# Kernel tuning notes

Hardware: AMD Instinct MI355X
Metric: run time of the kernel (lower is better)

Reference implementation:

```python
import jax, jax.numpy as jnp
import numpy as np
import math

N = 20000      # nodes
E = 320000     # edges
D = 256        # in_dim == out_dim (residual requires equality)
H = 8          # heads
K = D // H     # k_dim = 32
T = 3          # node types
R = 5          # edge (relation) types
C = 16         # output classes
SQRT_K = math.sqrt(K)


def setup_inputs() -> dict:
    key = jax.random.key(0)
    ks = jax.random.split(key, 18)
    x = jax.random.normal(ks[0], (N, D), jnp.float32)
    edge_index = jax.random.randint(ks[1], (2, E), 0, N, jnp.int32)
    node_type = jax.random.randint(ks[2], (N,), 0, T, jnp.int32)
    edge_type = jax.random.randint(ks[3], (E,), 0, R, jnp.int32)
    g_lin = math.sqrt(2.0 / (D + D))
    g_rel = math.sqrt(2.0 / (K + K))
    g_out = math.sqrt(2.0 / (D + C))
    Wk = jax.random.normal(ks[4], (T, D, D), jnp.float32) * g_lin
    bk = jnp.zeros((T, D), jnp.float32)
    Wq = jax.random.normal(ks[5], (T, D, D), jnp.float32) * g_lin
    bq = jnp.zeros((T, D), jnp.float32)
    Wv = jax.random.normal(ks[6], (T, D, D), jnp.float32) * g_lin
    bv = jnp.zeros((T, D), jnp.float32)
    Wa = jax.random.normal(ks[7], (T, D, D), jnp.float32) * g_lin
    ba = jnp.zeros((T, D), jnp.float32)
    rel_prior = jnp.ones((R, H), jnp.float32)
    rel_att = jax.random.normal(ks[8], (R, H, K, K), jnp.float32) * g_rel
    rel_msg = jax.random.normal(ks[9], (R, H, K, K), jnp.float32) * g_rel
    W_out = jax.random.normal(ks[10], (D, C), jnp.float32) * g_out
    b_out = jnp.zeros((C,), jnp.float32)
    return {"x": x, "edge_index": edge_index, "node_type": node_type,
            "edge_type": edge_type, "Wk": Wk, "bk": bk, "Wq": Wq, "bq": bq,
            "Wv": Wv, "bv": bv, "Wa": Wa, "ba": ba, "rel_prior": rel_prior,
            "rel_att": rel_att, "rel_msg": rel_msg, "W_out": W_out, "b_out": b_out}


def _typed_linear(h, W, b, node_type):
    # per-node-type Linear: small fixed loop over T types, masked select
    out = jnp.zeros((h.shape[0], W.shape[2]), h.dtype)
    for t in range(T):
        m = (node_type == t)[:, None]
        out = out + jnp.where(m, h @ W[t] + b[t], 0.0)
    return out


def _hgt_forward(x, edge_index, node_type, edge_type, Wk, bk, Wq, bq, Wv, bv,
                 Wa, ba, rel_prior, rel_att, rel_msg, W_out, b_out):
    src, dst = edge_index[0], edge_index[1]
    # typed projections -> [N, H, K]
    Kn = _typed_linear(x, Wk, bk, node_type).reshape(N, H, K)
    Qn = _typed_linear(x, Wq, bq, node_type).reshape(N, H, K)
    Vn = _typed_linear(x, Wv, bv, node_type).reshape(N, H, K)
    Ke, Qe, Ve = Kn[src], Qn[dst], Vn[src]  # [E, H, K] gathers
    # relation-specific bilinear transforms of K and V (fixed loop over R)
    Kt = jnp.zeros_like(Ke)
    Mt = jnp.zeros_like(Ve)
    for r in range(R):
        m = (edge_type == r)[:, None, None]
        Kt = Kt + jnp.where(m, jnp.einsum('ehk,hkl->ehl', Ke, rel_att[r]), 0.0)
        Mt = Mt + jnp.where(m, jnp.einsum('ehk,hkl->ehl', Ve, rel_msg[r]), 0.0)
    # attention logits with relation prior, scaled by sqrt(k_dim)
    logits = (Qe * Kt).sum(-1) * rel_prior[edge_type] / SQRT_K  # [E, H]
    # segment softmax over incoming edges per destination node
    mx = jax.ops.segment_max(logits, dst, num_segments=N)       # [N, H]
    ex = jnp.exp(logits - mx[dst])
    sm = jax.ops.segment_sum(ex, dst, num_segments=N)           # [N, H]
    att = ex / sm[dst]                                          # [E, H]
    # weighted messages, scatter-add aggregation
    msg = (Mt * att[:, :, None]).reshape(E, D)
    aggr = jax.ops.segment_sum(msg, dst, num_segments=N)        # [N, D]
    # update: ELU, typed output linear, residual
    h = jax.nn.elu(aggr)
    h = _typed_linear(h, Wa, ba, node_type) + x
    # final classifier + log_softmax
    return jax.nn.log_softmax(h @ W_out + b_out, axis=1)


def reference(x, edge_index, node_type, edge_type, Wk, bk, Wq, bq, Wv, bv,
              Wa, ba, rel_prior, rel_att, rel_msg, W_out, b_out):
    return _hgt_forward(x, edge_index, node_type, edge_type, Wk, bk, Wq, bq,
                        Wv, bv, Wa, ba, rel_prior, rel_att, rel_msg, W_out, b_out)
```

## Files before the change

### kernel.cpp

```cpp
#include <hip/hip_runtime.h>
#include <hip/hip_bf16.h>
#include <math.h>

#define NN 20000
#define NE 320000
#define DD 256
#define NH 8
#define KK 32
#define NR 5
#define NC 16
#define NB2 391
#define NPAD 20096

typedef unsigned short u16;
typedef unsigned int u32;
typedef __attribute__((ext_vector_type(8))) short bf16x8;
typedef __attribute__((ext_vector_type(4))) float f32x4;

__device__ __forceinline__ float bf2f(u16 v){ return __uint_as_float(((u32)v)<<16); }
__device__ __forceinline__ u16 f2bf(float f){
  u32 u = __float_as_uint(f);
  return (u16)((u + 0x7FFFu + ((u>>16)&1u)) >> 16);
}

__global__ void k_pre1(const int* __restrict__ ntype, const int* __restrict__ ei,
                       const int* __restrict__ etype, int* __restrict__ cnt,
                       int* __restrict__ off2, int* __restrict__ perm){
  int b = blockIdx.x;
  if(b < 79){
    int n = b*256 + threadIdx.x;
    int t = (n < NN) ? ntype[n] : -1;
    int lane = threadIdx.x & 63;
    #pragma unroll
    for(int tt=0; tt<3; tt++){
      unsigned long long mask = __ballot(t == tt);
      int leader = __ffsll((long long)mask) - 1;
      if(lane == leader) atomicAdd(&cnt[tt], __popcll(mask));
    }
  } else if(b < 1329){
    int e = (b-79)*256 + threadIdx.x;
    if(e < NE) atomicAdd(&off2[ei[NE + e]*NR + etype[e]], 1);
  } else {
    int i = (b-1329)*256 + threadIdx.x;
    if(i < NPAD) perm[i] = -1;
  }
}

__global__ __launch_bounds__(256) void k_pre2(int* __restrict__ off2, int* __restrict__ bsum,
                                              const int* __restrict__ cnt, int* __restrict__ boff){
  if(blockIdx.x == NB2){
    if(threadIdx.x == 0){
      int a = (cnt[0]+31)&~31;
      int bb = (cnt[1]+31)&~31;
      boff[0]=0; boff[1]=a; boff[2]=a+bb;
    }
    return;
  }
  __shared__ int sh[256];
  int t = threadIdx.x;
  int i = blockIdx.x*256 + t;
  int v = (i < NN*NR) ? off2[i] : 0;
  sh[t] = v;
  __syncthreads();
  for(int off=1; off<256; off<<=1){
    int val = (t >= off) ? sh[t-off] : 0;
    __syncthreads();
    sh[t] += val;
    __syncthreads();
  }
  if(i < NN*NR) off2[i] = sh[t] - v;
  if(t == 255) bsum[blockIdx.x] = sh[255];
}
__global__ __launch_bounds__(512) void k_scan2(int* __restrict__ bsum, int* __restrict__ off2){
  __shared__ int sh[512];
  int t = threadIdx.x;
  int v = (t < NB2) ? bsum[t] : 0;
  sh[t] = v;
  __syncthreads();
  for(int off=1; off<512; off<<=1){
    int val = (t >= off) ? sh[t-off] : 0;
    __syncthreads();
    sh[t] += val;
    __syncthreads();
  }
  if(t < NB2) bsum[t] = sh[t] - v;
  if(t == 511) off2[NN*NR] = sh[511];
}
__global__ void k_pre3(int* __restrict__ off2, const int* __restrict__ bsum,
                       const int* __restrict__ ntype, const int* __restrict__ boff,
                       int* __restrict__ bcur, int* __restrict__ perm,
                       int* __restrict__ pos2){
  int b = blockIdx.x;
  if(b < NB2){
    int i = b*256 + threadIdx.x;
    if(i < NN*NR) off2[i] += bsum[b];
  } else {
    int n = (b-NB2)*256 + threadIdx.x;
    int t = (n < NN) ? ntype[n] : -1;
    int lane = threadIdx.x & 63;
    #pragma unroll
    for(int tt=0; tt<3; tt++){
      unsigned long long mask = __ballot(t == tt);
      if(t == tt){
        int rank = __popcll(mask & ((1ull<<lane)-1ull));
        int leader = __ffsll((long long)mask) - 1;
        int base = 0;
        if(lane == leader) base = atomicAdd(&bcur[tt], __popcll(mask));
        base = __shfl(base, leader);
        int p = boff[tt] + base + rank;
        perm[p] = n;
        pos2[n] = p;
      }
    }
  }
}

__global__ __launch_bounds__(256) void k_work1(
    const int* __restrict__ ei, const int* __restrict__ etype,
    int* __restrict__ off2, int* __restrict__ packed,
    const int* __restrict__ pos2,
    const float* __restrict__ x, u16* __restrict__ xb,
    const float* __restrict__ Wk, const float* __restrict__ Wq,
    const float* __restrict__ Wv, const float* __restrict__ Wa,
    u16* __restrict__ Wtk, u16* __restrict__ Wtq,
    u16* __restrict__ Wtv, u16* __restrict__ Wta,
    const float* __restrict__ rmsg, const float* __restrict__ ratt,
    const float* __restrict__ prior, const float* __restrict__ Wo,
    u16* __restrict__ Mtm, u16* __restrict__ Atb, u16* __restrict__ Wot)
{
  __shared__ float tile[32][33];
  int b = blockIdx.x;
  if(b < 1250){
    int e = b*256 + threadIdx.x;
    if(e < NE){
      int pos = atomicAdd(&off2[ei[NE+e]*NR + etype[e]], 1);
      packed[pos] = pos2[ei[e]];
    }
  } else if(b < 3750){
    int i = (b-1250)*256 + threadIdx.x;
    float4 v0 = ((const float4*)x)[i*2+0];
    float4 v1 = ((const float4*)x)[i*2+1];
    uint4 o;
    o.x = (u32)f2bf(v0.x) | ((u32)f2bf(v0.y)<<16);
    o.y = (u32)f2bf(v0.z) | ((u32)f2bf(v0.w)<<16);
    o.z = (u32)f2bf(v1.x) | ((u32)f2bf(v1.y)<<16);
    o.w = (u32)f2bf(v1.z) | ((u32)f2bf(v1.w)<<16);
    ((uint4*)xb)[i] = o;
  } else if(b < 4518){
    int bp = b - 3750;
    int bx = bp & 7, by = (bp>>3) & 7, z = bp >> 6;
    int tensor = z/3, t = z%3;
    const float* W = (tensor==0) ? Wk : (tensor==1) ? Wq : (tensor==2) ? Wv : Wa;
    u16* O = (tensor==0) ? Wtk : (tensor==1) ? Wtq : (tensor==2) ? Wtv : Wta;
    int i0 = bx*32, j0 = by*32;
    int rr = threadIdx.x>>5, cc = threadIdx.x&31;
    #pragma unroll
    for(int p=0;p<4;p++)
      tile[rr+p*8][cc] = W[t*65536 + (i0+rr+p*8)*256 + j0+cc];
    __syncthreads();
    #pragma unroll
    for(int p=0;p<4;p++)
      O[t*65536 + (j0+rr+p*8)*256 + i0+cc] = f2bf(tile[cc][rr+p*8]);
  } else {
    int bp = b - 4518;
    if(bp < 160){
      int idx = bp*256 + threadIdx.x;
      int l = idx & 31, k = (idx >> 5) & 31, rh = idx >> 10;
      Mtm[(rh*32 + l)*32 + k] = f2bf(rmsg[idx]);
    } else if(bp < 320){
      int idx = (bp-160)*256 + threadIdx.x;
      int rh = idx >> 10;
      float scale = prior[rh] * 0.17677669529663687f;
      Atb[idx] = f2bf(ratt[idx] * scale);
    } else {
      int idx = (bp-320)*256 + threadIdx.x;
      int c = idx & 15, k = idx >> 4;
      Wot[c*DD + k] = f2bf(Wo[k*NC + c]);
    }
  }
}

#define XSP 264
__global__ __launch_bounds__(256) void k_projqa(
    const u16* __restrict__ xb, const int* __restrict__ perm, const int* __restrict__ boff,
    const u16* __restrict__ Wtk, const u16* __restrict__ Wtq, const u16* __restrict__ Wtv,
    const float* __restrict__ bk, const float* __restrict__ bq, const float* __restrict__ bv,
    u16* __restrict__ KVn, u16* __restrict__ Qn)
{
  __shared__ u16 smem[32*XSP];
  __shared__ int gids[32];
  int tid = threadIdx.x;
  int ts = (blockIdx.x >> 1)*32;
  int cb = (blockIdx.x & 1)*128;
  int t = (ts >= boff[2]) ? 2 : (ts >= boff[1]) ? 1 : 0;
  if(tid < 32) gids[tid] = perm[ts + tid];
  __syncthreads();
  #pragma unroll
  for(int it=0; it<4; it++){
    int q = tid + it*256;
    int row = q >> 5, c = q & 31;
    int g = gids[row];
    uint4 v = make_uint4(0,0,0,0);
    if(g >= 0) v = ((const uint4*)(xb + (size_t)g*DD))[c];
    ((uint4*)(smem + row*XSP))[c] = v;
  }
  __syncthreads();
  int lane = tid & 63;
  int w = tid >> 6;
  int quad = lane >> 4;
  int l16 = lane & 15;
  f32x4 accK[2][2], accQ[2][2], accV[2][2];
  #pragma unroll
  for(int mt=0;mt<2;mt++)
    #pragma unroll
    for(int nt=0;nt<2;nt++){
      accK[mt][nt]=(f32x4)(0.f); accQ[mt][nt]=(f32x4)(0.f); accV[mt][nt]=(f32x4)(0.f);
    }
  const u16* wkp = Wtk + (size_t)t*65536;
  const u16* wqp = Wtq + (size_t)t*65536;
  const u16* wvp = Wtv + (size_t)t*65536;
  #pragma unroll
  for(int kk=0; kk<8; kk++){
    int kb = kk*32 + quad*8;
    bf16x8 a0 = *(const bf16x8*)(smem + l16*XSP + kb);
    bf16x8 a1 = *(const bf16x8*)(smem + (16+l16)*XSP + kb);
    #pragma unroll
    for(int nt=0; nt<2; nt++){
      int n = cb + w*32 + nt*16 + l16;
      bf16x8 bK = *(const bf16x8*)(wkp + (size_t)n*DD + kb);
      bf16x8 bQ = *(const bf16x8*)(wqp + (size_t)n*DD + kb);
      bf16x8 bV = *(const bf16x8*)(wvp + (size_t)n*DD + kb);
      accK[0][nt] = __builtin_amdgcn_mfma_f32_16x16x32_bf16(a0, bK, accK[0][nt], 0,0,0);
      accK[1][nt] = __builtin_amdgcn_mfma_f32_16x16x32_bf16(a1, bK, accK[1][nt], 0,0,0);
      accQ[0][nt] = __builtin_amdgcn_mfma_f32_16x16x32_bf16(a0, bQ, accQ[0][nt], 0,0,0);
      accQ[1][nt] = __builtin_amdgcn_mfma_f32_16x16x32_bf16(a1, bQ, accQ[1][nt], 0,0,0);
      accV[0][nt] = __builtin_amdgcn_mfma_f32_16x16x32_bf16(a0, bV, accV[0][nt], 0,0,0);
      accV[1][nt] = __builtin_amdgcn_mfma_f32_16x16x32_bf16(a1, bV, accV[1][nt], 0,0,0);
    }
  }
  __syncthreads();
  #pragma unroll
  for(int nt=0; nt<2; nt++){
    int lc = w*32 + nt*16 + l16;
    int colg = cb + lc;
    int kvo = ((lc >> 2)*8 + (lc & 3));
    float bkv = bk[t*DD+colg], bvv = bv[t*DD+colg];
    #pragma unroll
    for(int mt=0; mt<2; mt++){
      #pragma unroll
      for(int reg=0; reg<4; reg++){
        int row = mt*16 + quad*4 + reg;
        smem[row*XSP + kvo]     = f2bf(accK[mt][nt][reg] + bkv);
        smem[row*XSP + kvo + 4] = f2bf(accV[mt][nt][reg] + bvv);
      }
    }
  }
  __syncthreads();
  #pragma unroll
  for(int it=0; it<4; it++){
    int q = tid + it*256;
    int row = q >> 5, c = q & 31;
    *(uint4*)(KVn + (size_t)(ts+row)*512 + (cb>>2)*8 + c*8) = ((uint4*)(smem + row*XSP))[c];
  }
  __syncthreads();
  #pragma unroll
  for(int nt=0; nt<2; nt++){
    int lc = w*32 + nt*16 + l16;
    float bqv = bq[t*DD + cb + lc];
    #pragma unroll
    for(int mt=0; mt<2; mt++){
      #pragma unroll
      for(int reg=0; reg<4; reg++){
        int row = mt*16 + quad*4 + reg;
        smem[row*XSP + lc] = f2bf(accQ[mt][nt][reg] + bqv);
      }
    }
  }
  __syncthreads();
  #pragma unroll
  for(int it=0; it<2; it++){
    int q = tid + it*256;
    int row = q >> 4, c = q & 15;
    *(uint4*)(Qn + (size_t)(ts+row)*DD + cb + c*8) = ((uint4*)(smem + row*XSP))[c];
  }
}

#define QSP 264
__global__ __launch_bounds__(256) void k_qa(
    const u16* __restrict__ Qn, const u16* __restrict__ Atb, u16* __restrict__ QA)
{
  __shared__ u16 qs[32*QSP];
  int tid = threadIdx.x;
  int tile = blockIdx.x / NR;
  int r = blockIdx.x - tile*NR;
  int ts = tile*32;
  #pragma unroll
  for(int it=0; it<4; it++){
    int q = tid + it*256;
    int row = q >> 5, c = q & 31;
    ((uint4*)(qs + row*QSP))[c] = ((const uint4*)(Qn + (size_t)(ts+row)*DD))[c];
  }
  __syncthreads();
  int lane = tid & 63, w = tid >> 6, quad = lane >> 4, l16 = lane & 15;
  f32x4 acc[2][2][2];
  #pragma unroll
  for(int hh=0;hh<2;hh++)
    #pragma unroll
    for(int mt=0;mt<2;mt++)
      #pragma unroll
      for(int nt=0;nt<2;nt++) acc[hh][mt][nt]=(f32x4)(0.f);
  #pragma unroll
  for(int hh=0; hh<2; hh++){
    int h = w*2 + hh;
    bf16x8 a0 = *(const bf16x8*)(qs + l16*QSP + h*32 + quad*8);
    bf16x8 a1 = *(const bf16x8*)(qs + (16+l16)*QSP + h*32 + quad*8);
    const u16* ap = Atb + (size_t)(r*NH + h)*1024;
    bf16x8 b0 = *(const bf16x8*)(ap + l16*32 + quad*8);
    bf16x8 b1 = *(const bf16x8*)(ap + (16+l16)*32 + quad*8);
    acc[hh][0][0] = __builtin_amdgcn_mfma_f32_16x16x32_bf16(a0, b0, acc[hh][0][0], 0,0,0);
    acc[hh][0][1] = __builtin_amdgcn_mfma_f32_16x16x32_bf16(a0, b1, acc[hh][0][1], 0,0,0);
    acc[hh][1][0] = __builtin_amdgcn_mfma_f32_16x16x32_bf16(a1, b0, acc[hh][1][0], 0,0,0);
    acc[hh][1][1] = __builtin_amdgcn_mfma_f32_16x16x32_bf16(a1, b1, acc[hh][1][1], 0,0,0);
  }
  __syncthreads();
  #pragma unroll
  for(int hh=0; hh<2; hh++){
    int h = w*2 + hh;
    #pragma unroll
    for(int mt=0; mt<2; mt++)
      #pragma unroll
      for(int nt=0; nt<2; nt++)
        #pragma unroll
        for(int reg=0; reg<4; reg++){
          int row = mt*16 + quad*4 + reg;
          qs[row*QSP + h*32 + nt*16 + l16] = f2bf(acc[hh][mt][nt][reg]);
        }
  }
  __syncthreads();
  #pragma unroll
  for(int it=0; it<4; it++){
    int q = tid + it*256;
    int row = q >> 5, c = q & 31;
    *(uint4*)(QA + ((size_t)(ts+row)*NR + r)*DD + c*8) = ((uint4*)(qs + row*QSP))[c];
  }
}

#define VSP 264
__global__ __launch_bounds__(256) void k_edge(
    const u16* __restrict__ KVn, const u16* __restrict__ QA,
    const int* __restrict__ off2, const int* __restrict__ packed,
    const int* __restrict__ perm, u16* __restrict__ aggrV)
{
  int lane = threadIdx.x & 63;
  int p = blockIdx.x*4 + (threadIdx.x >> 6);
  if(p >= NPAD) return;
  int n = perm[p];
  if(n < 0) return;
  int off = lane*4;
  float4 qa[NR];
  {
    const u16* qp = QA + (size_t)p*NR*DD + off;
    #pragma unroll
    for(int r=0;r<NR;r++){
      ushort4 q = *(const ushort4*)(qp + r*DD);
      qa[r] = make_float4(bf2f(q.x),bf2f(q.y),bf2f(q.z),bf2f(q.w));
    }
  }
  int eb[NR+1];
  eb[0] = (n==0) ? 0 : off2[n*NR - 1];
  #pragma unroll
  for(int i=1;i<=NR;i++) eb[i] = off2[n*NR + i - 1];
  float4 acc[NR];
  float s = 0.f;
  int lo8 = lane*8;

  #define EDGE_DOT(kv, q, dd) \
    { float k0=__uint_as_float((kv).x<<16), k1=__uint_as_float((kv).x&0xffff0000u); \
      float k2=__uint_as_float((kv).y<<16), k3=__uint_as_float((kv).y&0xffff0000u); \
      dd = k0*(q).x + k1*(q).y + k2*(q).z + k3*(q).w; }
  #define EDGE_ACC(kv, p, a) \
    { float v0=__uint_as_float((kv).z<<16), v1=__uint_as_float((kv).z&0xffff0000u); \
      float v2=__uint_as_float((kv).w<<16), v3=__uint_as_float((kv).w&0xffff0000u); \
      (a).x += (p)*v0; (a).y += (p)*v1; (a).z += (p)*v2; (a).w += (p)*v3; }
  #define RED3(d) { d += __shfl_xor(d,1); d += __shfl_xor(d,2); d += __shfl_xor(d,4); }

  #pragma unroll
  for(int r=0;r<NR;r++){
    float4 q = qa[r];
    float4 a = make_float4(0.f,0.f,0.f,0.f);
    int e = eb[r], end = eb[r+1];
    for(; e+4 <= end; e += 4){
      int s0 = packed[e], s1 = packed[e+1], s2 = packed[e+2], s3 = packed[e+3];
      uint4 kv0 = *(const uint4*)(KVn + (size_t)s0*512 + lo8);
      uint4 kv1 = *(const uint4*)(KVn + (size_t)s1*512 + lo8);
      uint4 kv2 = *(const uint4*)(KVn + (size_t)s2*512 + lo8);
      uint4 kv3 = *(const uint4*)(KVn + (size_t)s3*512 + lo8);
      float d0,d1,d2,d3;
      EDGE_DOT(kv0,q,d0); EDGE_DOT(kv1,q,d1); EDGE_DOT(kv2,q,d2); EDGE_DOT(kv3,q,d3);
      RED3(d0); RED3(d1); RED3(d2); RED3(d3);
      float p0=__expf(d0), p1=__expf(d1), p2=__expf(d2), p3=__expf(d3);
      s += p0 + p1 + p2 + p3;
      EDGE_ACC(kv0,p0,a); EDGE_ACC(kv1,p1,a); EDGE_ACC(kv2,p2,a); EDGE_ACC(kv3,p3,a);
    }
    if(e+2 <= end){
      int s0 = packed[e], s1 = packed[e+1];
      uint4 kv0 = *(const uint4*)(KVn + (size_t)s0*512 + lo8);
      uint4 kv1 = *(const uint4*)(KVn + (size_t)s1*512 + lo8);
      float d0,d1;
      EDGE_DOT(kv0,q,d0); EDGE_DOT(kv1,q,d1);
      RED3(d0); RED3(d1);
      float p0=__expf(d0), p1=__expf(d1);
      s += p0 + p1;
      EDGE_ACC(kv0,p0,a); EDGE_ACC(kv1,p1,a);
      e += 2;
    }
    if(e < end){
      int s0 = packed[e];
      uint4 kv0 = *(const uint4*)(KVn + (size_t)s0*512 + lo8);
      float d0;
      EDGE_DOT(kv0,q,d0);
      RED3(d0);
      float p0=__expf(d0);
      s += p0;
      EDGE_ACC(kv0,p0,a);
    }
    acc[r] = a;
  }
  #undef EDGE_DOT
  #undef EDGE_ACC
  #undef RED3
  float inv = (s > 0.f) ? (1.f/s) : 0.f;
  u16* op = aggrV + (size_t)p*NR*DD + off;
  #pragma unroll
  for(int r=0;r<NR;r++){
    ushort4 o;
    o.x=f2bf(acc[r].x*inv); o.y=f2bf(acc[r].y*inv);
    o.z=f2bf(acc[r].z*inv); o.w=f2bf(acc[r].w*inv);
    *(ushort4*)(op + r*DD) = o;
  }
}

__global__ __launch_bounds__(256) void k_mo(
    const u16* __restrict__ aggrV, const u16* __restrict__ Mtm,
    const float* __restrict__ x,
    const int* __restrict__ perm, const int* __restrict__ boff,
    const u16* __restrict__ Wta, const float* __restrict__ ba,
    const u16* __restrict__ Wot, const float* __restrict__ bo,
    float* __restrict__ out)
{
  __shared__ u16 Vs[32*VSP];
  __shared__ u16 hs[32*VSP];
  __shared__ u16 h2s[32*VSP];
  __shared__ int gids[32];
  int tid = threadIdx.x;
  int ts = blockIdx.x*32;
  int t = (ts >= boff[2]) ? 2 : (ts >= boff[1]) ? 1 : 0;
  if(tid < 32) gids[tid] = perm[ts + tid];
  __syncthreads();
  int lane = tid & 63, w = tid >> 6, quad = lane >> 4, l16 = lane & 15;

  f32x4 macc[2][2][2];
  #pragma unroll
  for(int hh=0;hh<2;hh++)
    #pragma unroll
    for(int mt=0;mt<2;mt++)
      #pragma unroll
      for(int nt=0;nt<2;nt++) macc[hh][mt][nt]=(f32x4)(0.f);
  #pragma unroll
  for(int r=0;r<NR;r++){
    u16* B = (r & 1) ? h2s : Vs;
    #pragma unroll
    for(int it=0; it<4; it++){
      int q = tid + it*256;
      int row = q >> 5, c = q & 31;
      ((uint4*)(B + row*VSP))[c] =
        ((const uint4*)(aggrV + ((size_t)(ts+row)*NR + r)*DD))[c];
    }
    __syncthreads();
    #pragma unroll
    for(int hh=0; hh<2; hh++){
      int h = w*2 + hh;
      bf16x8 a0 = *(const bf16x8*)(B + l16*VSP + h*32 + quad*8);
      bf16x8 a1 = *(const bf16x8*)(B + (16+l16)*VSP + h*32 + quad*8);
      const u16* mp = Mtm + ((size_t)(r*NH + h)*32)*32;
      bf16x8 b0 = *(const bf16x8*)(mp + l16*32 + quad*8);
      bf16x8 b1 = *(const bf16x8*)(mp + (16+l16)*32 + quad*8);
      macc[hh][0][0] = __builtin_amdgcn_mfma_f32_16x16x32_bf16(a0, b0, macc[hh][0][0], 0,0,0);
      macc[hh][0][1] = __builtin_amdgcn_mfma_f32_16x16x32_bf16(a0, b1, macc[hh][0][1], 0,0,0);
      macc[hh][1][0] = __builtin_amdgcn_mfma_f32_16x16x32_bf16(a1, b0, macc[hh][1][0], 0,0,0);
      macc[hh][1][1] = __builtin_amdgcn_mfma_f32_16x16x32_bf16(a1, b1, macc[hh][1][1], 0,0,0);
    }
  }
  #pragma unroll
  for(int hh=0; hh<2; hh++){
    int h = w*2 + hh;
    #pragma unroll
    for(int mt=0; mt<2; mt++){
      #pragma unroll
      for(int nt=0; nt<2; nt++){
        #pragma unroll
        for(int reg=0; reg<4; reg++){
          int row = mt*16 + quad*4 + reg;
          float v = macc[hh][mt][nt][reg];
          v = (v > 0.f) ? v : expm1f(v);
          hs[row*VSP + h*32 + nt*16 + l16] = f2bf(v);
        }
      }
    }
  }
  __syncthreads();

  f32x4 acc[2][4];
  #pragma unroll
  for(int mt=0;mt<2;mt++)
    #pragma unroll
    for(int nt=0;nt<4;nt++) acc[mt][nt]=(f32x4)(0.f);
  const u16* wap = Wta + (size_t)t*65536;
  #pragma unroll
  for(int kk=0; kk<8; kk++){
    int kb = kk*32 + quad*8;
    bf16x8 a0 = *(const bf16x8*)(hs + l16*VSP + kb);
    bf16x8 a1 = *(const bf16x8*)(hs + (16+l16)*VSP + kb);
    #pragma unroll
    for(int nt=0; nt<4; nt++){
      int n = w*64 + nt*16 + l16;
      bf16x8 b = *(const bf16x8*)(wap + (size_t)n*DD + kb);
      acc[0][nt] = __builtin_amdgcn_mfma_f32_16x16x32_bf16(a0, b, acc[0][nt], 0,0,0);
      acc[1][nt] = __builtin_amdgcn_mfma_f32_16x16x32_bf16(a1, b, acc[1][nt], 0,0,0);
    }
  }
  #pragma unroll
  for(int nt=0; nt<4; nt++){
    int colg = w*64 + nt*16 + l16;
    float bav = ba[t*DD + colg];
    #pragma unroll
    for(int mt=0; mt<2; mt++){
      #pragma unroll
      for(int reg=0; reg<4; reg++){
        int row = mt*16 + quad*4 + reg;
        int g = gids[row];
        float xr = (g>=0) ? x[(size_t)g*DD + colg] : 0.f;
        h2s[row*VSP + colg] = f2bf(acc[mt][nt][reg] + bav + xr);
      }
    }
  }
  __syncthreads();
  if(w < 2){
    f32x4 cacc = (f32x4)(0.f);
    #pragma unroll
    for(int kk=0; kk<8; kk++){
      int kb = kk*32 + quad*8;
      bf16x8 a = *(const bf16x8*)(h2s + (w*16 + l16)*VSP + kb);
      bf16x8 b = *(const bf16x8*)(Wot + (size_t)l16*DD + kb);
      cacc = __builtin_amdgcn_mfma_f32_16x16x32_bf16(a, b, cacc, 0,0,0);
    }
    float bov = bo[l16];
    #pragma unroll
    for(int reg=0; reg<4; reg++){
      int row = w*16 + quad*4 + reg;
      int g = gids[row];
      float v = cacc[reg] + bov;
      float m = v;
      m = fmaxf(m, __shfl_xor(m,1)); m = fmaxf(m, __shfl_xor(m,2));
      m = fmaxf(m, __shfl_xor(m,4)); m = fmaxf(m, __shfl_xor(m,8));
      float p = __expf(v - m);
      p += __shfl_xor(p,1); p += __shfl_xor(p,2);
      p += __shfl_xor(p,4); p += __shfl_xor(p,8);
      float lse = m + __logf(p);
      if(g >= 0) out[(size_t)g*NC + l16] = v - lse;
    }
  }
}

extern "C" void kernel_launch(void* const* d_in, const int* in_sizes, int n_in,
                              void* d_out, int out_size, void* d_ws, size_t ws_size,
                              hipStream_t stream)
{
  const float* x     = (const float*)d_in[0];
  const int*   ei    = (const int*)d_in[1];
  const int*   ntype = (const int*)d_in[2];
  const int*   etype = (const int*)d_in[3];
  const float* Wk    = (const float*)d_in[4];
  const float* bk    = (const float*)d_in[5];
  const float* Wq    = (const float*)d_in[6];
  const float* bq    = (const float*)d_in[7];
  const float* Wv    = (const float*)d_in[8];
  const float* bv    = (const float*)d_in[9];
  const float* Wa    = (const float*)d_in[10];
  const float* ba    = (const float*)d_in[11];
  const float* prior = (const float*)d_in[12];
  const float* ratt  = (const float*)d_in[13];
  const float* rmsg  = (const float*)d_in[14];
  const float* Wo    = (const float*)d_in[15];
  const float* bo    = (const float*)d_in[16];
  float* out = (float*)d_out;

  char* ws = (char*)d_ws;
  int* iw      = (int*)ws;
  int* cnt     = iw + 0;
  int* bcur    = iw + 4;
  int* boff    = iw + 8;
  int* off2    = iw + 16;
  int* perm    = iw + 100032;
  int* packed  = iw + 120128;
  int* bsum    = iw + 440128;
  int* pos2    = iw + 440640;

  size_t fb = 1842688;
  u16*   KVn   = (u16*)(ws + fb);   fb += 2ull*NPAD*512;
  u16*   Qn    = (u16*)(ws + fb);   fb += 2ull*NPAD*DD;
  u16*   QA    = (u16*)(ws + fb);   fb += 2ull*NPAD*NR*DD;
  u16*   aggrV = (u16*)(ws + fb);   fb += 2ull*NPAD*NR*DD;
  u16*   Wtk   = (u16*)(ws + fb);   fb += 2ull*3*65536;
  u16*   Wtq   = (u16*)(ws + fb);   fb += 2ull*3*65536;
  u16*   Wtv   = (u16*)(ws + fb);   fb += 2ull*3*65536;
  u16*   Wta   = (u16*)(ws + fb);   fb += 2ull*3*65536;
  u16*   Wot   = (u16*)(ws + fb);   fb += 2ull*NC*DD;
  u16*   Mtm   = (u16*)(ws + fb);   fb += 2ull*NR*NH*KK*KK;
  u16*   Atb   = (u16*)(ws + fb);   fb += 2ull*NR*NH*KK*KK;
  u16* xb = aggrV;

  hipMemsetAsync(iw, 0, (size_t)(16 + NN*NR + 1)*sizeof(int), stream);

  k_pre1   <<<1408, 256, 0, stream>>>(ntype, ei, etype, cnt, off2, perm);
  k_pre2   <<<NB2+1, 256, 0, stream>>>(off2, bsum, cnt, boff);
  k_scan2  <<<1, 512, 0, stream>>>(bsum, off2);
  k_pre3   <<<NB2+79, 256, 0, stream>>>(off2, bsum, ntype, boff, bcur, perm, pos2);
  k_work1  <<<4854, 256, 0, stream>>>(ei, etype, off2, packed, pos2, x, xb,
                                      Wk, Wq, Wv, Wa, Wtk, Wtq, Wtv, Wta,
                                      rmsg, ratt, prior, Wo, Mtm, Atb, Wot);
  k_projqa <<<1256, 256, 0, stream>>>(xb, perm, boff, Wtk, Wtq, Wtv, bk, bq, bv,
                                      KVn, Qn);
  k_qa     <<<628*NR, 256, 0, stream>>>(Qn, Atb, QA);
  k_edge   <<<5024, 256, 0, stream>>>(KVn, QA, off2, packed, perm, aggrV);
  k_mo     <<<628, 256, 0, stream>>>(aggrV, Mtm, x, perm, boff, Wta, ba, Wot, bo, out);
}
```

Measured before the change: 305.3 us.

## Split each node's relation groups across two wavefronts in edge kernel

The edge attention kernel now assigns each destination node to a 128-thread block of two wavefronts instead of one wavefront. The five relation segments are divided at the split point that best balances edge counts, and each wavefront processes its share. The per-head softmax denominators are then combined through shared memory with a block barrier. The aim is to raise parallelism and the number of gathers in flight per node, shortening per-node latency. The cost is a barrier, a small shared-memory reduction and twice as many waves, some of which may get little work.

Result: no change. 306.9 us (+0.5%).

```diff
diff --git a/kernel.cpp b/kernel.cpp
--- a/kernel.cpp
+++ b/kernel.cpp
@@ -345,101 +345,121 @@
   }
 }
 
-#define VSP 264
-__global__ __launch_bounds__(256) void k_edge(
+__global__ __launch_bounds__(128) void k_edge(
     const u16* __restrict__ KVn, const u16* __restrict__ QA,
     const int* __restrict__ off2, const int* __restrict__ packed,
     const int* __restrict__ perm, u16* __restrict__ aggrV)
 {
+  __shared__ float sh_s[2][8];
   int lane = threadIdx.x & 63;
-  int p = blockIdx.x*4 + (threadIdx.x >> 6);
-  if(p >= NPAD) return;
+  int z = threadIdx.x >> 6;
+  int h = lane >> 3;
+  int p = blockIdx.x;
   int n = perm[p];
   if(n < 0) return;
   int off = lane*4;
-  float4 qa[NR];
-  {
-    const u16* qp = QA + (size_t)p*NR*DD + off;
-    #pragma unroll
-    for(int r=0;r<NR;r++){
-      ushort4 q = *(const ushort4*)(qp + r*DD);
-      qa[r] = make_float4(bf2f(q.x),bf2f(q.y),bf2f(q.z),bf2f(q.w));
-    }
-  }
   int eb[NR+1];
   eb[0] = (n==0) ? 0 : off2[n*NR - 1];
   #pragma unroll
   for(int i=1;i<=NR;i++) eb[i] = off2[n*NR + i - 1];
-  float4 acc[NR];
+  int total = eb[NR] - eb[0];
+  int rsplit = 1;
+  int best;
+  { int d = 2*(eb[1]-eb[0]) - total; best = d<0 ? -d : d; }
+  #pragma unroll
+  for(int rr=2; rr<=4; rr++){
+    int d = 2*(eb[rr]-eb[0]) - total; d = d<0 ? -d : d;
+    if(d < best){ best = d; rsplit = rr; }
+  }
   float s = 0.f;
   int lo8 = lane*8;
+  float4 a0 = make_float4(0.f,0.f,0.f,0.f), a1 = a0, a2 = a0, a3 = a0, a4 = a0;
 
   #define EDGE_DOT(kv, q, dd) \
     { float k0=__uint_as_float((kv).x<<16), k1=__uint_as_float((kv).x&0xffff0000u); \
       float k2=__uint_as_float((kv).y<<16), k3=__uint_as_float((kv).y&0xffff0000u); \
       dd = k0*(q).x + k1*(q).y + k2*(q).z + k3*(q).w; }
-  #define EDGE_ACC(kv, p, a) \
+  #define EDGE_ACC(kv, pw, a) \
     { float v0=__uint_as_float((kv).z<<16), v1=__uint_as_float((kv).z&0xffff0000u); \
       float v2=__uint_as_float((kv).w<<16), v3=__uint_as_float((kv).w&0xffff0000u); \
-      (a).x += (p)*v0; (a).y += (p)*v1; (a).z += (p)*v2; (a).w += (p)*v3; }
+      (a).x += (pw)*v0; (a).y += (pw)*v1; (a).z += (pw)*v2; (a).w += (pw)*v3; }
   #define RED3(d) { d += __shfl_xor(d,1); d += __shfl_xor(d,2); d += __shfl_xor(d,4); }
 
-  #pragma unroll
-  for(int r=0;r<NR;r++){
-    float4 q = qa[r];
-    float4 a = make_float4(0.f,0.f,0.f,0.f);
-    int e = eb[r], end = eb[r+1];
-    for(; e+4 <= end; e += 4){
-      int s0 = packed[e], s1 = packed[e+1], s2 = packed[e+2], s3 = packed[e+3];
-      uint4 kv0 = *(const uint4*)(KVn + (size_t)s0*512 + lo8);
-      uint4 kv1 = *(const uint4*)(KVn + (size_t)s1*512 + lo8);
-      uint4 kv2 = *(const uint4*)(KVn + (size_t)s2*512 + lo8);
-      uint4 kv3 = *(const uint4*)(KVn + (size_t)s3*512 + lo8);
-      float d0,d1,d2,d3;
-      EDGE_DOT(kv0,q,d0); EDGE_DOT(kv1,q,d1); EDGE_DOT(kv2,q,d2); EDGE_DOT(kv3,q,d3);
-      RED3(d0); RED3(d1); RED3(d2); RED3(d3);
-      float p0=__expf(d0), p1=__expf(d1), p2=__expf(d2), p3=__expf(d3);
-      s += p0 + p1 + p2 + p3;
-      EDGE_ACC(kv0,p0,a); EDGE_ACC(kv1,p1,a); EDGE_ACC(kv2,p2,a); EDGE_ACC(kv3,p3,a);
-    }
-    if(e+2 <= end){
-      int s0 = packed[e], s1 = packed[e+1];
-      uint4 kv0 = *(const uint4*)(KVn + (size_t)s0*512 + lo8);
-      uint4 kv1 = *(const uint4*)(KVn + (size_t)s1*512 + lo8);
-      float d0,d1;
-      EDGE_DOT(kv0,q,d0); EDGE_DOT(kv1,q,d1);
-      RED3(d0); RED3(d1);
-      float p0=__expf(d0), p1=__expf(d1);
-      s += p0 + p1;
-      EDGE_ACC(kv0,p0,a); EDGE_ACC(kv1,p1,a);
-      e += 2;
-    }
-    if(e < end){
-      int s0 = packed[e];
-      uint4 kv0 = *(const uint4*)(KVn + (size_t)s0*512 + lo8);
-      float d0;
-      EDGE_DOT(kv0,q,d0);
-      RED3(d0);
-      float p0=__expf(d0);
-      s += p0;
-      EDGE_ACC(kv0,p0,a);
-    }
-    acc[r] = a;
-  }
+  #define PROC(rr, av) \
+  if((rr < rsplit) == (z == 0)){ \
+    ushort4 qu = *(const ushort4*)(QA + ((size_t)p*NR + rr)*DD + off); \
+    float4 q = make_float4(bf2f(qu.x),bf2f(qu.y),bf2f(qu.z),bf2f(qu.w)); \
+    float4 a = make_float4(0.f,0.f,0.f,0.f); \
+    int e = eb[rr], end = eb[rr+1]; \
+    for(; e+4 <= end; e += 4){ \
+      int s0 = packed[e], s1 = packed[e+1], s2 = packed[e+2], s3 = packed[e+3]; \
+      uint4 kv0 = *(const uint4*)(KVn + (size_t)s0*512 + lo8); \
+      uint4 kv1 = *(const uint4*)(KVn + (size_t)s1*512 + lo8); \
+      uint4 kv2 = *(const uint4*)(KVn + (size_t)s2*512 + lo8); \
+      uint4 kv3 = *(const uint4*)(KVn + (size_t)s3*512 + lo8); \
+      float d0,d1,d2,d3; \
+      EDGE_DOT(kv0,q,d0); EDGE_DOT(kv1,q,d1); EDGE_DOT(kv2,q,d2); EDGE_DOT(kv3,q,d3); \
+      RED3(d0); RED3(d1); RED3(d2); RED3(d3); \
+      float p0=__expf(d0), p1=__expf(d1), p2=__expf(d2), p3=__expf(d3); \
+      s += p0 + p1 + p2 + p3; \
+      EDGE_ACC(kv0,p0,a); EDGE_ACC(kv1,p1,a); EDGE_ACC(kv2,p2,a); EDGE_ACC(kv3,p3,a); \
+    } \
+    if(e+2 <= end){ \
+      int s0 = packed[e], s1 = packed[e+1]; \
+      uint4 kv0 = *(const uint4*)(KVn + (size_t)s0*512 + lo8); \
+      uint4 kv1 = *(const uint4*)(KVn + (size_t)s1*512 + lo8); \
+      float d0,d1; \
+      EDGE_DOT(kv0,q,d0); EDGE_DOT(kv1,q,d1); \
+      RED3(d0); RED3(d1); \
+      float p0=__expf(d0), p1=__expf(d1); \
+      s += p0 + p1; \
+      EDGE_ACC(kv0,p0,a); EDGE_ACC(kv1,p1,a); \
+      e += 2; \
+    } \
+    if(e < end){ \
+      int s0 = packed[e]; \
+      uint4 kv0 = *(const uint4*)(KVn + (size_t)s0*512 + lo8); \
+      float d0; \
+      EDGE_DOT(kv0,q,d0); \
+      RED3(d0); \
+      float p0=__expf(d0); \
+      s += p0; \
+      EDGE_ACC(kv0,p0,a); \
+    } \
+    av = a; \
+  }
+
+  PROC(0,a0)
+  PROC(1,a1)
+  PROC(2,a2)
+  PROC(3,a3)
+  PROC(4,a4)
+  #undef PROC
   #undef EDGE_DOT
   #undef EDGE_ACC
   #undef RED3
-  float inv = (s > 0.f) ? (1.f/s) : 0.f;
+
+  if((lane & 7) == 0) sh_s[z][h] = s;
+  __syncthreads();
+  float stot = sh_s[0][h] + sh_s[1][h];
+  float inv = (stot > 0.f) ? (1.f/stot) : 0.f;
   u16* op = aggrV + (size_t)p*NR*DD + off;
-  #pragma unroll
-  for(int r=0;r<NR;r++){
-    ushort4 o;
-    o.x=f2bf(acc[r].x*inv); o.y=f2bf(acc[r].y*inv);
-    o.z=f2bf(acc[r].z*inv); o.w=f2bf(acc[r].w*inv);
-    *(ushort4*)(op + r*DD) = o;
-  }
-}
-
+  #define STORE(rr, av) \
+  if((rr < rsplit) == (z == 0)){ \
+    ushort4 o; \
+    o.x=f2bf((av).x*inv); o.y=f2bf((av).y*inv); \
+    o.z=f2bf((av).z*inv); o.w=f2bf((av).w*inv); \
+    *(ushort4*)(op + rr*DD) = o; \
+  }
+  STORE(0,a0)
+  STORE(1,a1)
+  STORE(2,a2)
+  STORE(3,a3)
+  STORE(4,a4)
+  #undef STORE
+}
+
+#define VSP 264
 __global__ __launch_bounds__(256) void k_mo(
     const u16* __restrict__ aggrV, const u16* __restrict__ Mtm,
     const float* __restrict__ x,
@@ -632,6 +652,6 @@
   k_projqa <<<1256, 256, 0, stream>>>(xb, perm, boff, Wtk, Wtq, Wtv, bk, bq, bv,
                                       KVn, Qn);
   k_qa     <<<628*NR, 256, 0, stream>>>(Qn, Atb, QA);
-  k_edge   <<<5024, 256, 0, stream>>>(KVn, QA, off2, packed, perm, aggrV);
+  k_edge   <<<NPAD, 128, 0, stream>>>(KVn, QA, off2, packed, perm, aggrV);
   k_mo     <<<628, 256, 0, stream>>>(aggrV, Mtm, x, perm, boff, Wta, ba, Wot, bo, out);
 }
```

## Fuse relation-attention Q transform into edge kernel and defer softmax normalization

Applied to the files above, without the earlier changes.

The separate k_qa kernel, which wrote a per-node, per-relation QA tensor to global memory, is folded into k_edge. Each block now computes 16 nodes' QA rows per relation with MFMA into shared memory and then runs the edge loop on them. The softmax denominator is written as a per-head inverse to a new sinv buffer, and k_mo applies it while loading aggrV, which removes the QA write/read round trip and one launch. In exchange, each k_edge wave handles four nodes serially with a block barrier per relation. That may reduce parallelism and latency hiding in the gather loop, and it adds a scale pass in k_mo.

New measurement: 323.9 us. 1.06x slower.

```diff
diff --git a/kernel.cpp b/kernel.cpp
--- a/kernel.cpp
+++ b/kernel.cpp
@@ -21,6 +21,11 @@
 __device__ __forceinline__ u16 f2bf(float f){
   u32 u = __float_as_uint(f);
   return (u16)((u + 0x7FFFu + ((u>>16)&1u)) >> 16);
+}
+__device__ __forceinline__ u32 scale2(u32 w, float iv){
+  float lo = bf2f((u16)(w & 0xffffu)) * iv;
+  float hi = bf2f((u16)(w >> 16)) * iv;
+  return (u32)f2bf(lo) | ((u32)f2bf(hi) << 16);
 }
 
 __global__ void k_pre1(const int* __restrict__ ntype, const int* __restrict__ ei,
@@ -286,176 +291,158 @@
 }
 
 #define QSP 264
-__global__ __launch_bounds__(256) void k_qa(
-    const u16* __restrict__ Qn, const u16* __restrict__ Atb, u16* __restrict__ QA)
+__global__ __launch_bounds__(256) void k_edge(
+    const u16* __restrict__ Qn, const u16* __restrict__ Atb,
+    const u16* __restrict__ KVn,
+    const int* __restrict__ off2, const int* __restrict__ packed,
+    const int* __restrict__ perm, u16* __restrict__ aggrV,
+    float* __restrict__ sinv)
 {
-  __shared__ u16 qs[32*QSP];
+  __shared__ u16 qs[16*QSP];
+  __shared__ u16 qas[16*QSP];
+  __shared__ int gids[16];
   int tid = threadIdx.x;
-  int tile = blockIdx.x / NR;
-  int r = blockIdx.x - tile*NR;
-  int ts = tile*32;
-  #pragma unroll
-  for(int it=0; it<4; it++){
-    int q = tid + it*256;
-    int row = q >> 5, c = q & 31;
+  int ts = blockIdx.x*16;
+  if(tid < 16) gids[tid] = perm[ts + tid];
+  #pragma unroll
+  for(int it=0; it<2; it++){
+    int qq = tid + it*256;
+    int row = qq >> 5, c = qq & 31;
     ((uint4*)(qs + row*QSP))[c] = ((const uint4*)(Qn + (size_t)(ts+row)*DD))[c];
   }
   __syncthreads();
   int lane = tid & 63, w = tid >> 6, quad = lane >> 4, l16 = lane & 15;
-  f32x4 acc[2][2][2];
-  #pragma unroll
-  for(int hh=0;hh<2;hh++)
-    #pragma unroll
-    for(int mt=0;mt<2;mt++)
-      #pragma unroll
-      for(int nt=0;nt<2;nt++) acc[hh][mt][nt]=(f32x4)(0.f);
-  #pragma unroll
-  for(int hh=0; hh<2; hh++){
-    int h = w*2 + hh;
-    bf16x8 a0 = *(const bf16x8*)(qs + l16*QSP + h*32 + quad*8);
-    bf16x8 a1 = *(const bf16x8*)(qs + (16+l16)*QSP + h*32 + quad*8);
-    const u16* ap = Atb + (size_t)(r*NH + h)*1024;
-    bf16x8 b0 = *(const bf16x8*)(ap + l16*32 + quad*8);
-    bf16x8 b1 = *(const bf16x8*)(ap + (16+l16)*32 + quad*8);
-    acc[hh][0][0] = __builtin_amdgcn_mfma_f32_16x16x32_bf16(a0, b0, acc[hh][0][0], 0,0,0);
-    acc[hh][0][1] = __builtin_amdgcn_mfma_f32_16x16x32_bf16(a0, b1, acc[hh][0][1], 0,0,0);
-    acc[hh][1][0] = __builtin_amdgcn_mfma_f32_16x16x32_bf16(a1, b0, acc[hh][1][0], 0,0,0);
-    acc[hh][1][1] = __builtin_amdgcn_mfma_f32_16x16x32_bf16(a1, b1, acc[hh][1][1], 0,0,0);
-  }
-  __syncthreads();
-  #pragma unroll
-  for(int hh=0; hh<2; hh++){
-    int h = w*2 + hh;
-    #pragma unroll
-    for(int mt=0; mt<2; mt++)
-      #pragma unroll
-      for(int nt=0; nt<2; nt++)
-        #pragma unroll
-        for(int reg=0; reg<4; reg++){
-          int row = mt*16 + quad*4 + reg;
-          qs[row*QSP + h*32 + nt*16 + l16] = f2bf(acc[hh][mt][nt][reg]);
-        }
-  }
-  __syncthreads();
-  #pragma unroll
-  for(int it=0; it<4; it++){
-    int q = tid + it*256;
-    int row = q >> 5, c = q & 31;
-    *(uint4*)(QA + ((size_t)(ts+row)*NR + r)*DD + c*8) = ((uint4*)(qs + row*QSP))[c];
-  }
-}
-
-#define VSP 264
-__global__ __launch_bounds__(256) void k_edge(
-    const u16* __restrict__ KVn, const u16* __restrict__ QA,
-    const int* __restrict__ off2, const int* __restrict__ packed,
-    const int* __restrict__ perm, u16* __restrict__ aggrV)
-{
-  int lane = threadIdx.x & 63;
-  int p = blockIdx.x*4 + (threadIdx.x >> 6);
-  if(p >= NPAD) return;
-  int n = perm[p];
-  if(n < 0) return;
-  int off = lane*4;
-  float4 qa[NR];
-  {
-    const u16* qp = QA + (size_t)p*NR*DD + off;
-    #pragma unroll
-    for(int r=0;r<NR;r++){
-      ushort4 q = *(const ushort4*)(qp + r*DD);
-      qa[r] = make_float4(bf2f(q.x),bf2f(q.y),bf2f(q.z),bf2f(q.w));
-    }
-  }
-  int eb[NR+1];
-  eb[0] = (n==0) ? 0 : off2[n*NR - 1];
-  #pragma unroll
-  for(int i=1;i<=NR;i++) eb[i] = off2[n*NR + i - 1];
-  float4 acc[NR];
-  float s = 0.f;
-  int lo8 = lane*8;
-
-  #define EDGE_DOT(kv, q, dd) \
+  int off = lane*4, lo8 = lane*8;
+  float sAcc[4] = {0.f, 0.f, 0.f, 0.f};
+
+  #define EDGE_DOT(kv, qv, dd) \
     { float k0=__uint_as_float((kv).x<<16), k1=__uint_as_float((kv).x&0xffff0000u); \
       float k2=__uint_as_float((kv).y<<16), k3=__uint_as_float((kv).y&0xffff0000u); \
-      dd = k0*(q).x + k1*(q).y + k2*(q).z + k3*(q).w; }
-  #define EDGE_ACC(kv, p, a) \
+      dd = k0*(qv).x + k1*(qv).y + k2*(qv).z + k3*(qv).w; }
+  #define EDGE_ACC(kv, pw, a) \
     { float v0=__uint_as_float((kv).z<<16), v1=__uint_as_float((kv).z&0xffff0000u); \
       float v2=__uint_as_float((kv).w<<16), v3=__uint_as_float((kv).w&0xffff0000u); \
-      (a).x += (p)*v0; (a).y += (p)*v1; (a).z += (p)*v2; (a).w += (p)*v3; }
+      (a).x += (pw)*v0; (a).y += (pw)*v1; (a).z += (pw)*v2; (a).w += (pw)*v3; }
   #define RED3(d) { d += __shfl_xor(d,1); d += __shfl_xor(d,2); d += __shfl_xor(d,4); }
 
-  #pragma unroll
-  for(int r=0;r<NR;r++){
-    float4 q = qa[r];
-    float4 a = make_float4(0.f,0.f,0.f,0.f);
-    int e = eb[r], end = eb[r+1];
-    for(; e+4 <= end; e += 4){
-      int s0 = packed[e], s1 = packed[e+1], s2 = packed[e+2], s3 = packed[e+3];
-      uint4 kv0 = *(const uint4*)(KVn + (size_t)s0*512 + lo8);
-      uint4 kv1 = *(const uint4*)(KVn + (size_t)s1*512 + lo8);
-      uint4 kv2 = *(const uint4*)(KVn + (size_t)s2*512 + lo8);
-      uint4 kv3 = *(const uint4*)(KVn + (size_t)s3*512 + lo8);
-      float d0,d1,d2,d3;
-      EDGE_DOT(kv0,q,d0); EDGE_DOT(kv1,q,d1); EDGE_DOT(kv2,q,d2); EDGE_DOT(kv3,q,d3);
-      RED3(d0); RED3(d1); RED3(d2); RED3(d3);
-      float p0=__expf(d0), p1=__expf(d1), p2=__expf(d2), p3=__expf(d3);
-      s += p0 + p1 + p2 + p3;
-      EDGE_ACC(kv0,p0,a); EDGE_ACC(kv1,p1,a); EDGE_ACC(kv2,p2,a); EDGE_ACC(kv3,p3,a);
-    }
-    if(e+2 <= end){
-      int s0 = packed[e], s1 = packed[e+1];
-      uint4 kv0 = *(const uint4*)(KVn + (size_t)s0*512 + lo8);
-      uint4 kv1 = *(const uint4*)(KVn + (size_t)s1*512 + lo8);
-      float d0,d1;
-      EDGE_DOT(kv0,q,d0); EDGE_DOT(kv1,q,d1);
-      RED3(d0); RED3(d1);
-      float p0=__expf(d0), p1=__expf(d1);
-      s += p0 + p1;
-      EDGE_ACC(kv0,p0,a); EDGE_ACC(kv1,p1,a);
-      e += 2;
-    }
-    if(e < end){
-      int s0 = packed[e];
-      uint4 kv0 = *(const uint4*)(KVn + (size_t)s0*512 + lo8);
-      float d0;
-      EDGE_DOT(kv0,q,d0);
-      RED3(d0);
-      float p0=__expf(d0);
-      s += p0;
-      EDGE_ACC(kv0,p0,a);
-    }
-    acc[r] = a;
+  for(int r=0; r<NR; r++){
+    if(r > 0) __syncthreads();
+    {
+      f32x4 acc[2][2];
+      #pragma unroll
+      for(int hh=0;hh<2;hh++)
+        #pragma unroll
+        for(int nt=0;nt<2;nt++) acc[hh][nt]=(f32x4)(0.f);
+      #pragma unroll
+      for(int hh=0; hh<2; hh++){
+        int h = w*2 + hh;
+        bf16x8 a0 = *(const bf16x8*)(qs + l16*QSP + h*32 + quad*8);
+        const u16* ap = Atb + (size_t)(r*NH + h)*1024;
+        bf16x8 b0 = *(const bf16x8*)(ap + l16*32 + quad*8);
+        bf16x8 b1 = *(const bf16x8*)(ap + (16+l16)*32 + quad*8);
+        acc[hh][0] = __builtin_amdgcn_mfma_f32_16x16x32_bf16(a0, b0, acc[hh][0], 0,0,0);
+        acc[hh][1] = __builtin_amdgcn_mfma_f32_16x16x32_bf16(a0, b1, acc[hh][1], 0,0,0);
+      }
+      #pragma unroll
+      for(int hh=0; hh<2; hh++){
+        int h = w*2 + hh;
+        #pragma unroll
+        for(int nt=0; nt<2; nt++)
+          #pragma unroll
+          for(int reg=0; reg<4; reg++){
+            int row = quad*4 + reg;
+            qas[row*QSP + h*32 + nt*16 + l16] = f2bf(acc[hh][nt][reg]);
+          }
+      }
+    }
+    __syncthreads();
+    #pragma unroll
+    for(int i=0; i<4; i++){
+      int row = w*4 + i;
+      int n = gids[row];
+      if(n < 0) continue;
+      int idx = n*NR + r;
+      int e = (idx == 0) ? 0 : off2[idx-1];
+      int end = off2[idx];
+      ushort4 qu = *(const ushort4*)(qas + row*QSP + off);
+      float4 qv = make_float4(bf2f(qu.x),bf2f(qu.y),bf2f(qu.z),bf2f(qu.w));
+      float4 a = make_float4(0.f,0.f,0.f,0.f);
+      float s = 0.f;
+      for(; e+4 <= end; e += 4){
+        int s0 = packed[e], s1 = packed[e+1], s2 = packed[e+2], s3 = packed[e+3];
+        uint4 kv0 = *(const uint4*)(KVn + (size_t)s0*512 + lo8);
+        uint4 kv1 = *(const uint4*)(KVn + (size_t)s1*512 + lo8);
+        uint4 kv2 = *(const uint4*)(KVn + (size_t)s2*512 + lo8);
+        uint4 kv3 = *(const uint4*)(KVn + (size_t)s3*512 + lo8);
+        float d0,d1,d2,d3;
+        EDGE_DOT(kv0,qv,d0); EDGE_DOT(kv1,qv,d1); EDGE_DOT(kv2,qv,d2); EDGE_DOT(kv3,qv,d3);
+        RED3(d0); RED3(d1); RED3(d2); RED3(d3);
+        float p0=__expf(d0), p1=__expf(d1), p2=__expf(d2), p3=__expf(d3);
+        s += p0 + p1 + p2 + p3;
+        EDGE_ACC(kv0,p0,a); EDGE_ACC(kv1,p1,a); EDGE_ACC(kv2,p2,a); EDGE_ACC(kv3,p3,a);
+      }
+      if(e+2 <= end){
+        int s0 = packed[e], s1 = packed[e+1];
+        uint4 kv0 = *(const uint4*)(KVn + (size_t)s0*512 + lo8);
+        uint4 kv1 = *(const uint4*)(KVn + (size_t)s1*512 + lo8);
+        float d0,d1;
+        EDGE_DOT(kv0,qv,d0); EDGE_DOT(kv1,qv,d1);
+        RED3(d0); RED3(d1);
+        float p0=__expf(d0), p1=__expf(d1);
+        s += p0 + p1;
+        EDGE_ACC(kv0,p0,a); EDGE_ACC(kv1,p1,a);
+        e += 2;
+      }
+      if(e < end){
+        int s0 = packed[e];
+        uint4 kv0 = *(const uint4*)(KVn + (size_t)s0*512 + lo8);
+        float d0;
+        EDGE_DOT(kv0,qv,d0);
+        RED3(d0);
+        float p0=__expf(d0);
+        s += p0;
+        EDGE_ACC(kv0,p0,a);
+      }
+      sAcc[i] += s;
+      ushort4 o;
+      o.x=f2bf(a.x); o.y=f2bf(a.y); o.z=f2bf(a.z); o.w=f2bf(a.w);
+      *(ushort4*)(aggrV + ((size_t)(ts+row)*NR + r)*DD + off) = o;
+    }
   }
   #undef EDGE_DOT
   #undef EDGE_ACC
   #undef RED3
-  float inv = (s > 0.f) ? (1.f/s) : 0.f;
-  u16* op = aggrV + (size_t)p*NR*DD + off;
-  #pragma unroll
-  for(int r=0;r<NR;r++){
-    ushort4 o;
-    o.x=f2bf(acc[r].x*inv); o.y=f2bf(acc[r].y*inv);
-    o.z=f2bf(acc[r].z*inv); o.w=f2bf(acc[r].w*inv);
-    *(ushort4*)(op + r*DD) = o;
-  }
-}
-
+  #pragma unroll
+  for(int i=0; i<4; i++){
+    int row = w*4 + i;
+    int n = gids[row];
+    if(n >= 0 && (lane & 7) == 0){
+      float sv = sAcc[i];
+      sinv[(size_t)(ts+row)*8 + (lane>>3)] = (sv > 0.f) ? (1.f/sv) : 0.f;
+    }
+  }
+}
+
+#define VSP 264
 __global__ __launch_bounds__(256) void k_mo(
     const u16* __restrict__ aggrV, const u16* __restrict__ Mtm,
     const float* __restrict__ x,
     const int* __restrict__ perm, const int* __restrict__ boff,
     const u16* __restrict__ Wta, const float* __restrict__ ba,
     const u16* __restrict__ Wot, const float* __restrict__ bo,
+    const float* __restrict__ sinv,
     float* __restrict__ out)
 {
   __shared__ u16 Vs[32*VSP];
   __shared__ u16 hs[32*VSP];
   __shared__ u16 h2s[32*VSP];
   __shared__ int gids[32];
+  __shared__ float sInvS[256];
   int tid = threadIdx.x;
   int ts = blockIdx.x*32;
   int t = (ts >= boff[2]) ? 2 : (ts >= boff[1]) ? 1 : 0;
   if(tid < 32) gids[tid] = perm[ts + tid];
+  sInvS[tid] = sinv[(size_t)ts*8 + tid];
   __syncthreads();
   int lane = tid & 63, w = tid >> 6, quad = lane >> 4, l16 = lane & 15;
 
@@ -473,8 +460,12 @@
     for(int it=0; it<4; it++){
       int q = tid + it*256;
       int row = q >> 5, c = q & 31;
-      ((uint4*)(B + row*VSP))[c] =
-        ((const uint4*)(aggrV + ((size_t)(ts+row)*NR + r)*DD))[c];
+      float iv = sInvS[row*8 + (c>>2)];
+      uint4 v = ((const uint4*)(aggrV + ((size_t)(ts+row)*NR + r)*DD))[c];
+      uint4 o;
+      o.x = scale2(v.x, iv); o.y = scale2(v.y, iv);
+      o.z = scale2(v.z, iv); o.w = scale2(v.w, iv);
+      ((uint4*)(B + row*VSP))[c] = o;
     }
     __syncthreads();
     #pragma unroll
@@ -605,11 +596,11 @@
   int* packed  = iw + 120128;
   int* bsum    = iw + 440128;
   int* pos2    = iw + 440640;
-
-  size_t fb = 1842688;
+  float* sinv  = (float*)(iw + 460640);
+
+  size_t fb = 2485760;
   u16*   KVn   = (u16*)(ws + fb);   fb += 2ull*NPAD*512;
   u16*   Qn    = (u16*)(ws + fb);   fb += 2ull*NPAD*DD;
-  u16*   QA    = (u16*)(ws + fb);   fb += 2ull*NPAD*NR*DD;
   u16*   aggrV = (u16*)(ws + fb);   fb += 2ull*NPAD*NR*DD;
   u16*   Wtk   = (u16*)(ws + fb);   fb += 2ull*3*65536;
   u16*   Wtq   = (u16*)(ws + fb);   fb += 2ull*3*65536;
@@ -631,7 +622,6 @@
                                       rmsg, ratt, prior, Wo, Mtm, Atb, Wot);
   k_projqa <<<1256, 256, 0, stream>>>(xb, perm, boff, Wtk, Wtq, Wtv, bk, bq, bv,
                                       KVn, Qn);
-  k_qa     <<<628*NR, 256, 0, stream>>>(Qn, Atb, QA);
-  k_edge   <<<5024, 256, 0, stream>>>(KVn, QA, off2, packed, perm, aggrV);
-  k_mo     <<<628, 256, 0, stream>>>(aggrV, Mtm, x, perm, boff, Wta, ba, Wot, bo, out);
-}
+  k_edge   <<<1256, 256, 0, stream>>>(Qn, Atb, KVn, off2, packed, perm, aggrV, sinv);
+  k_mo     <<<628, 256, 0, stream>>>(aggrV, Mtm, x, perm, boff, Wta, ba, Wot, bo, sinv, out);
+}
```
